# Performance work log

Measured on AMD Instinct MI355X. Metric: run time of the kernel, lower is better.

Reference implementation:

```python
import jax, jax.numpy as jnp
import numpy as np

HIDDEN = 1024
N_HEAD = 16
D_HEAD = HIDDEN // N_HEAD


def setup_inputs() -> dict:
    key = jax.random.key(0)
    k1, k2, k3, k4, k5, k6, k7 = jax.random.split(key, 7)
    B, Sq, Sk = 8, 1024, 1024
    decoder_input = jax.random.normal(k1, (B, Sq, HIDDEN), dtype=jnp.float32)
    encoder_output = jax.random.normal(k2, (B, Sk, HIDDEN), dtype=jnp.float32)
    # torch.rand -> uniform [0,1) for the per-head projection params
    W_query = jax.random.uniform(k3, (N_HEAD, D_HEAD, HIDDEN), dtype=jnp.float32)
    W_key = jax.random.uniform(k4, (N_HEAD, D_HEAD, HIDDEN), dtype=jnp.float32)
    W_value = jax.random.uniform(k5, (N_HEAD, D_HEAD, HIDDEN), dtype=jnp.float32)
    # nn.Linear default init: U(-1/sqrt(fan_in), 1/sqrt(fan_in))
    bound = 1.0 / np.sqrt(HIDDEN)
    W_out = jax.random.uniform(k6, (HIDDEN, HIDDEN), dtype=jnp.float32, minval=-bound, maxval=bound)
    b_out = jax.random.uniform(k7, (HIDDEN,), dtype=jnp.float32, minval=-bound, maxval=bound)
    return {
        "decoder_input": decoder_input,
        "encoder_output": encoder_output,
        "W_query": W_query,
        "W_key": W_key,
        "W_value": W_value,
        "W_out": W_out,
        "b_out": b_out,
    }


def reference(decoder_input, encoder_output, W_query, W_key, W_value, W_out, b_out):
    # per-head projections, vectorized over heads: x @ W[i].T == einsum over hidden
    q = jnp.einsum("bqh,ndh->bnqd", decoder_input, W_query)   # [B,N,Sq,D]
    k = jnp.einsum("bkh,ndh->bnkd", encoder_output, W_key)    # [B,N,Sk,D]
    v = jnp.einsum("bkh,ndh->bnkd", encoder_output, W_value)  # [B,N,Sk,D]
    scores = jnp.einsum("bnqd,bnkd->bnqk", q, k) / jnp.sqrt(jnp.float32(D_HEAD))
    attn = jax.nn.softmax(scores, axis=-1)                     # [B,N,Sq,Sk]
    heads = jnp.einsum("bnqk,bnkd->bnqd", attn, v)             # [B,N,Sq,D]
    B, N, Sq, D = heads.shape
    concat = jnp.transpose(heads, (0, 2, 1, 3)).reshape(B, Sq, N * D)  # [B,Sq,H]
    out = concat @ W_out.T + b_out
    return out
```

## Files before the change

### kernel.cpp

```cpp
#include <hip/hip_runtime.h>
#include <math.h>

#define HID 1024
#define NH 16
#define DH 64
#define BATCH 8
#define SEQ 1024
#define MTOT (BATCH * SEQ)

typedef __attribute__((ext_vector_type(8))) short bfrag;
typedef __attribute__((ext_vector_type(4))) float f32x4;
typedef __attribute__((ext_vector_type(8))) unsigned short us8;
typedef __attribute__((ext_vector_type(4))) unsigned short us4;
typedef unsigned int u32;
typedef unsigned short u16;

__device__ __forceinline__ u16 f2b(float f) {
    u32 u = __float_as_uint(f);
    return (u16)((u + 0x7FFFu + ((u >> 16) & 1u)) >> 16);
}
__device__ __forceinline__ float b2f(u16 h) { return __uint_as_float(((u32)h) << 16); }

__device__ __forceinline__ void gl_lds16(const void* g, void* l) {
    __builtin_amdgcn_global_load_lds(
        (const __attribute__((address_space(1))) unsigned int*)g,
        (__attribute__((address_space(3))) unsigned int*)l, 16, 0, 0);
}

__device__ __forceinline__ u32 swz(u32 L) { return L ^ (((L >> 6) & 7u) << 4); }
__device__ __forceinline__ u32 unswz(u32 p) {
    u32 b = ((((p >> 6) ^ (p >> 8)) & 1u) << 4) | (((p >> 7) & 1u) << 5) | (((p >> 8) & 1u) << 6);
    return p ^ b;
}

__global__ __launch_bounds__(256) void split_w(const float* __restrict__ x,
                                               u16* __restrict__ hi, u16* __restrict__ lo, int n4) {
    int i = blockIdx.x * blockDim.x + threadIdx.x;
    int stride = gridDim.x * blockDim.x;
    for (; i < n4; i += stride) {
        float4 f = ((const float4*)x)[i];
        float v[4] = {f.x, f.y, f.z, f.w};
        us4 h, l;
#pragma unroll
        for (int j = 0; j < 4; ++j) {
            u16 hh = f2b(v[j]);
            h[j] = hh;
            l[j] = f2b(v[j] - b2f(hh));
        }
        ((us4*)hi)[i] = h;
        ((us4*)lo)[i] = l;
    }
}
__global__ __launch_bounds__(256) void cvt_w(const float* __restrict__ x, u16* __restrict__ hi, int n4) {
    int i = blockIdx.x * blockDim.x + threadIdx.x;
    int stride = gridDim.x * blockDim.x;
    for (; i < n4; i += stride) {
        float4 f = ((const float4*)x)[i];
        us4 h;
        h[0] = f2b(f.x); h[1] = f2b(f.y); h[2] = f2b(f.z); h[3] = f2b(f.w);
        ((us4*)hi)[i] = h;
    }
}

template <int TERMS, int XMODE, int OMODE>
__global__ __launch_bounds__(256) void gemm_mfma(
    const float* __restrict__ Xf, const u16* __restrict__ Xb,
    const u16* __restrict__ Wh, const u16* __restrict__ Wl,
    const float* __restrict__ bias, float* __restrict__ Of, u16* __restrict__ Ob) {
    constexpr u32 OFF_AH = 0, OFF_BH = 8192, OFF_AL = 16384, OFF_BL = 24576;
    __shared__ __align__(16) char smem[(TERMS == 3) ? 32768 : 16384];

    u32 bid = blockIdx.x;
    u32 wg = (bid & 7) * 64 + (bid >> 3);
    const u32 m0 = (wg >> 3) * 128, n0 = (wg & 7) * 128;

    const int tid = threadIdx.x;
    const int w = tid >> 6, lane = tid & 63, c = lane & 15, g = lane >> 4;
    const int wr = w >> 1, wc = w & 1;

    u32 pa[4], pb[4];
#pragma unroll
    for (int i = 0; i < 4; ++i) {
        pa[i] = swz((u32)(wr * 64 + i * 16 + c) * 64 + (u32)g * 16);
        pb[i] = swz((u32)(wc * 64 + i * 16 + c) * 64 + (u32)g * 16);
    }

    f32x4 acc[4][4];
#pragma unroll
    for (int i = 0; i < 4; ++i)
#pragma unroll
        for (int j = 0; j < 4; ++j) acc[i][j] = f32x4{0.f, 0.f, 0.f, 0.f};

    for (int kb = 0; kb < HID / 32; ++kb) {
        const int koff = kb * 32;
        {
            const int nW = (TERMS == 3) ? 16 : 8;
            const int total = nW + ((XMODE == 1) ? 8 : 0);
            for (int id = w; id < total; id += 4) {
                u32 p = (u32)(id & 7) * 1024 + (u32)lane * 16;
                u32 L = unswz(p);
                u32 row = L >> 6, colb = L & 63;
                const char* src;
                u32 loff;
                if (id < 8) {
                    src = (const char*)Wh + ((size_t)(n0 + row)) * 2048 + (size_t)koff * 2 + colb;
                    loff = OFF_BH + (p & 0xFFFFFC00u);
                } else if (TERMS == 3 && id < 16) {
                    src = (const char*)Wl + ((size_t)(n0 + row)) * 2048 + (size_t)koff * 2 + colb;
                    loff = OFF_BL + (p & 0xFFFFFC00u);
                } else {
                    src = (const char*)Xb + ((size_t)(m0 + row)) * 2048 + (size_t)koff * 2 + colb;
                    loff = OFF_AH + (p & 0xFFFFFC00u);
                }
                gl_lds16(src, smem + loff);
            }
        }
        if (XMODE == 0) {
            const int row = tid >> 1, half = tid & 1;
            const float* xr = Xf + ((size_t)(m0 + row)) * HID + koff + half * 16;
            float4 f0 = ((const float4*)xr)[0], f1 = ((const float4*)xr)[1],
                   f2 = ((const float4*)xr)[2], f3 = ((const float4*)xr)[3];
            float v[16] = {f0.x, f0.y, f0.z, f0.w, f1.x, f1.y, f1.z, f1.w,
                           f2.x, f2.y, f2.z, f2.w, f3.x, f3.y, f3.z, f3.w};
#pragma unroll
            for (int s = 0; s < 2; ++s) {
                us8 h, l8;
#pragma unroll
                for (int i = 0; i < 8; ++i) {
                    u16 hh = f2b(v[s * 8 + i]);
                    h[i] = hh;
                    if (TERMS == 3) l8[i] = f2b(v[s * 8 + i] - b2f(hh));
                }
                u32 ph = swz((u32)row * 64 + (u32)half * 32 + (u32)s * 16);
                *(us8*)(smem + OFF_AH + ph) = h;
                if (TERMS == 3) *(us8*)(smem + OFF_AL + ph) = l8;
            }
        }
        __syncthreads();
        bfrag ah[4], al[4];
#pragma unroll
        for (int mi = 0; mi < 4; ++mi) {
            ah[mi] = *(const bfrag*)(smem + OFF_AH + pa[mi]);
            if (TERMS == 3) al[mi] = *(const bfrag*)(smem + OFF_AL + pa[mi]);
        }
#pragma unroll
        for (int ni = 0; ni < 4; ++ni) {
            bfrag bh = *(const bfrag*)(smem + OFF_BH + pb[ni]);
            bfrag bl;
            if (TERMS == 3) bl = *(const bfrag*)(smem + OFF_BL + pb[ni]);
#pragma unroll
            for (int mi = 0; mi < 4; ++mi) {
                acc[mi][ni] = __builtin_amdgcn_mfma_f32_16x16x32_bf16(ah[mi], bh, acc[mi][ni], 0, 0, 0);
                if (TERMS == 3) {
                    acc[mi][ni] = __builtin_amdgcn_mfma_f32_16x16x32_bf16(ah[mi], bl, acc[mi][ni], 0, 0, 0);
                    acc[mi][ni] = __builtin_amdgcn_mfma_f32_16x16x32_bf16(al[mi], bh, acc[mi][ni], 0, 0, 0);
                }
            }
        }
        __syncthreads();
    }
#pragma unroll
    for (int mi = 0; mi < 4; ++mi) {
#pragma unroll
        for (int ni = 0; ni < 4; ++ni) {
            const u32 n = n0 + wc * 64 + ni * 16 + c;
            float bv = (OMODE == 2) ? bias[n] : 0.f;
#pragma unroll
            for (int r = 0; r < 4; ++r) {
                const size_t m = m0 + wr * 64 + mi * 16 + 4 * g + r;
                float val = acc[mi][ni][r] + bv;
                if (OMODE == 1) Ob[m * HID + n] = f2b(val);
                else Of[m * HID + n] = val;
            }
        }
    }
}

__global__ __launch_bounds__(256) void attn_mfma(
    const float* __restrict__ Qf, const float* __restrict__ Kf,
    const u16* __restrict__ Vb, u16* __restrict__ Cc) {
    __shared__ __align__(16) u16 Qh[64 * 72], Ql[64 * 72], KP[64 * 72], KV[64 * 72];

    u32 bid = blockIdx.x;
    u32 wg = (bid & 7) * 256 + (bid >> 3);
    const int b = wg >> 8;
    const int head = (wg >> 4) & 15;
    const int q0 = (wg & 15) * 64;

    const int tid = threadIdx.x;
    const int w = tid >> 6, lane = tid & 63, c = lane & 15, g = lane >> 4;

    {
        const int row = tid >> 2, cs = tid & 3;
        const float* qr = Qf + ((size_t)(b * SEQ + q0 + row)) * HID + head * DH + cs * 16;
        float4 f0 = ((const float4*)qr)[0], f1 = ((const float4*)qr)[1],
               f2 = ((const float4*)qr)[2], f3 = ((const float4*)qr)[3];
        float v[16] = {f0.x, f0.y, f0.z, f0.w, f1.x, f1.y, f1.z, f1.w,
                       f2.x, f2.y, f2.z, f2.w, f3.x, f3.y, f3.z, f3.w};
#pragma unroll
        for (int s = 0; s < 2; ++s) {
            us8 h, l8;
#pragma unroll
            for (int i = 0; i < 8; ++i) {
                u16 hh = f2b(v[s * 8 + i]);
                h[i] = hh;
                l8[i] = f2b(v[s * 8 + i] - b2f(hh));
            }
            *(us8*)(Qh + row * 72 + cs * 16 + s * 8) = h;
            *(us8*)(Ql + row * 72 + cs * 16 + s * 8) = l8;
        }
    }

    float m_[4] = {-1e30f, -1e30f, -1e30f, -1e30f};
    float l_[4] = {0.f, 0.f, 0.f, 0.f};
    f32x4 acc[4];
#pragma unroll
    for (int j = 0; j < 4; ++j) acc[j] = f32x4{0.f, 0.f, 0.f, 0.f};

    for (int kc = 0; kc < SEQ / 64; ++kc) {
        __syncthreads();
        {
            const int row = tid >> 2, cs = tid & 3;
            const float* kr = Kf + ((size_t)(b * SEQ + kc * 64 + row)) * HID + head * DH + cs * 16;
            float4 f0 = ((const float4*)kr)[0], f1 = ((const float4*)kr)[1],
                   f2 = ((const float4*)kr)[2], f3 = ((const float4*)kr)[3];
            float v[16] = {f0.x, f0.y, f0.z, f0.w, f1.x, f1.y, f1.z, f1.w,
                           f2.x, f2.y, f2.z, f2.w, f3.x, f3.y, f3.z, f3.w};
#pragma unroll
            for (int s = 0; s < 2; ++s) {
                us8 h, l8;
#pragma unroll
                for (int i = 0; i < 8; ++i) {
                    u16 hh = f2b(v[s * 8 + i]);
                    h[i] = hh;
                    l8[i] = f2b(v[s * 8 + i] - b2f(hh));
                }
                *(us8*)(KP + row * 72 + cs * 16 + s * 8) = h;
                *(us8*)(KV + row * 72 + cs * 16 + s * 8) = l8;
            }
        }
        __syncthreads();
        f32x4 s4[4];
#pragma unroll
        for (int j = 0; j < 4; ++j) s4[j] = f32x4{0.f, 0.f, 0.f, 0.f};
#pragma unroll
        for (int ks = 0; ks < 2; ++ks) {
            bfrag ah = *(const bfrag*)(Qh + (w * 16 + c) * 72 + ks * 32 + g * 8);
            bfrag al = *(const bfrag*)(Ql + (w * 16 + c) * 72 + ks * 32 + g * 8);
#pragma unroll
            for (int jf = 0; jf < 4; ++jf) {
                bfrag bh = *(const bfrag*)(KP + (jf * 16 + c) * 72 + ks * 32 + g * 8);
                bfrag bl = *(const bfrag*)(KV + (jf * 16 + c) * 72 + ks * 32 + g * 8);
                s4[jf] = __builtin_amdgcn_mfma_f32_16x16x32_bf16(ah, bh, s4[jf], 0, 0, 0);
                s4[jf] = __builtin_amdgcn_mfma_f32_16x16x32_bf16(ah, bl, s4[jf], 0, 0, 0);
                s4[jf] = __builtin_amdgcn_mfma_f32_16x16x32_bf16(al, bh, s4[jf], 0, 0, 0);
            }
        }
        __syncthreads();
        float scl[4];
#pragma unroll
        for (int r = 0; r < 4; ++r) {
            float v0 = s4[0][r] * 0.125f, v1 = s4[1][r] * 0.125f,
                  v2 = s4[2][r] * 0.125f, v3 = s4[3][r] * 0.125f;
            float rm = fmaxf(fmaxf(v0, v1), fmaxf(v2, v3));
            rm = fmaxf(rm, __shfl_xor(rm, 1));
            rm = fmaxf(rm, __shfl_xor(rm, 2));
            rm = fmaxf(rm, __shfl_xor(rm, 4));
            rm = fmaxf(rm, __shfl_xor(rm, 8));
            float mn = fmaxf(m_[r], rm);
            scl[r] = __expf(m_[r] - mn);
            float p0 = __expf(v0 - mn), p1 = __expf(v1 - mn),
                  p2 = __expf(v2 - mn), p3 = __expf(v3 - mn);
            float rs = p0 + p1 + p2 + p3;
            rs += __shfl_xor(rs, 1);
            rs += __shfl_xor(rs, 2);
            rs += __shfl_xor(rs, 4);
            rs += __shfl_xor(rs, 8);
            l_[r] = l_[r] * scl[r] + rs;
            m_[r] = mn;
            const int prow = (w * 16 + 4 * g + r) * 72;
            KP[prow + 0 + c] = f2b(p0);
            KP[prow + 16 + c] = f2b(p1);
            KP[prow + 32 + c] = f2b(p2);
            KP[prow + 48 + c] = f2b(p3);
        }
#pragma unroll
        for (int jd = 0; jd < 4; ++jd) {
            f32x4 t = acc[jd];
            t[0] *= scl[0]; t[1] *= scl[1]; t[2] *= scl[2]; t[3] *= scl[3];
            acc[jd] = t;
        }
#pragma unroll
        for (int it = 0; it < 2; ++it) {
            const int idx = tid + it * 256;
            const int k = idx >> 3, ds = idx & 7, d0 = ds * 8;
            const u16* vr = Vb + ((size_t)(b * SEQ + kc * 64 + k)) * HID + head * DH + d0;
            us8 vv = *(const us8*)vr;
            const u32 kg = (((u32)(k >> 3)) ^ ((u32)ds & 3u)) << 3;
#pragma unroll
            for (int i = 0; i < 8; ++i) KV[(d0 + i) * 72 + kg + (k & 7)] = vv[i];
        }
        __syncthreads();
#pragma unroll
        for (int ks = 0; ks < 2; ++ks) {
            bfrag ap = *(const bfrag*)(KP + (w * 16 + c) * 72 + ks * 32 + g * 8);
#pragma unroll
            for (int jd = 0; jd < 4; ++jd) {
                const int d = jd * 16 + c;
                const u32 G = (u32)(ks * 4 + g);
                const u32 key = (u32)((d >> 3) & 3);
                bfrag bv = *(const bfrag*)(KV + d * 72 + ((G ^ key) << 3));
                acc[jd] = __builtin_amdgcn_mfma_f32_16x16x32_bf16(ap, bv, acc[jd], 0, 0, 0);
            }
        }
    }
    float inv[4] = {1.f / l_[0], 1.f / l_[1], 1.f / l_[2], 1.f / l_[3]};
#pragma unroll
    for (int jd = 0; jd < 4; ++jd) {
#pragma unroll
        for (int r = 0; r < 4; ++r) {
            Cc[((size_t)(b * SEQ + q0 + w * 16 + 4 * g + r)) * HID + head * DH + jd * 16 + c] =
                f2b(acc[jd][r] * inv[r]);
        }
    }
}

extern "C" void kernel_launch(void* const* d_in, const int* in_sizes, int n_in,
                              void* d_out, int out_size, void* d_ws, size_t ws_size,
                              hipStream_t stream) {
    const float* dec = (const float*)d_in[0];
    const float* enc = (const float*)d_in[1];
    const float* Wq = (const float*)d_in[2];
    const float* Wk = (const float*)d_in[3];
    const float* Wv = (const float*)d_in[4];
    const float* Wo = (const float*)d_in[5];
    const float* bo = (const float*)d_in[6];
    float* out = (float*)d_out;

    char* ws = (char*)d_ws;
    float* Qf = (float*)ws;
    float* Kf = (float*)(ws + (size_t)(32u << 20));
    u16* Vb = (u16*)(ws + (size_t)(64u << 20));
    u16* Cc = (u16*)(ws + (size_t)(80u << 20));
    u16* Wqh = (u16*)(ws + (size_t)(96u << 20));
    u16* Wql = Wqh + (1u << 20);
    u16* Wkh = Wql + (1u << 20);
    u16* Wkl = Wkh + (1u << 20);
    u16* Wvh = Wkl + (1u << 20);
    u16* Woh = Wvh + (1u << 20);

    const int n4w = HID * HID / 4;
    split_w<<<512, 256, 0, stream>>>(Wq, Wqh, Wql, n4w);
    split_w<<<512, 256, 0, stream>>>(Wk, Wkh, Wkl, n4w);
    cvt_w<<<512, 256, 0, stream>>>(Wv, Wvh, n4w);
    cvt_w<<<512, 256, 0, stream>>>(Wo, Woh, n4w);

    gemm_mfma<3, 0, 0><<<512, 256, 0, stream>>>(dec, nullptr, Wqh, Wql, nullptr, Qf, nullptr);
    gemm_mfma<3, 0, 0><<<512, 256, 0, stream>>>(enc, nullptr, Wkh, Wkl, nullptr, Kf, nullptr);
    gemm_mfma<1, 0, 1><<<512, 256, 0, stream>>>(enc, nullptr, Wvh, nullptr, nullptr, nullptr, Vb);

    attn_mfma<<<2048, 256, 0, stream>>>(Qf, Kf, Vb, Cc);

    gemm_mfma<1, 1, 2><<<512, 256, 0, stream>>>(nullptr, Cc, Woh, nullptr, bo, out, nullptr);
}
```

Before: 488.7 us.

## Emit head-major bf16 hi/lo Q/K and transposed V from projection epilogues

The Q and K projection epilogues now write bf16 hi/lo pairs in a [B,H,S,D] layout, with the softmax scale and log2e folded into Q. V is written pre-transposed as [B,H,D,S]. The attention kernel loads all tiles with direct global-to-LDS copies under an XOR swizzle, drops the per-tile fp32 split and V transpose, uses exp2, and removes two barriers per iteration. The weight conversion kernels are merged into one prep kernel, which also converts the encoder input to bf16 for the V GEMM. This cuts attention-side global traffic and ALU work, but adds strided scattered epilogue stores and an extra encoder conversion pass.

```diff
diff --git a/kernel.cpp b/kernel.cpp
--- a/kernel.cpp
+++ b/kernel.cpp
@@ -15,6 +15,8 @@
 typedef unsigned int u32;
 typedef unsigned short u16;
 
+#define SCALE_Q 0.18033688011112042f
+
 __device__ __forceinline__ u16 f2b(float f) {
     u32 u = __float_as_uint(f);
     return (u16)((u + 0x7FFFu + ((u >> 16) & 1u)) >> 16);
@@ -32,41 +34,55 @@
     u32 b = ((((p >> 6) ^ (p >> 8)) & 1u) << 4) | (((p >> 7) & 1u) << 5) | (((p >> 8) & 1u) << 6);
     return p ^ b;
 }
-
-__global__ __launch_bounds__(256) void split_w(const float* __restrict__ x,
-                                               u16* __restrict__ hi, u16* __restrict__ lo, int n4) {
-    int i = blockIdx.x * blockDim.x + threadIdx.x;
-    int stride = gridDim.x * blockDim.x;
-    for (; i < n4; i += stride) {
-        float4 f = ((const float4*)x)[i];
-        float v[4] = {f.x, f.y, f.z, f.w};
-        us4 h, l;
-#pragma unroll
-        for (int j = 0; j < 4; ++j) {
-            u16 hh = f2b(v[j]);
-            h[j] = hh;
-            l[j] = f2b(v[j] - b2f(hh));
-        }
-        ((us4*)hi)[i] = h;
-        ((us4*)lo)[i] = l;
-    }
-}
-__global__ __launch_bounds__(256) void cvt_w(const float* __restrict__ x, u16* __restrict__ hi, int n4) {
-    int i = blockIdx.x * blockDim.x + threadIdx.x;
-    int stride = gridDim.x * blockDim.x;
-    for (; i < n4; i += stride) {
-        float4 f = ((const float4*)x)[i];
-        us4 h;
-        h[0] = f2b(f.x); h[1] = f2b(f.y); h[2] = f2b(f.z); h[3] = f2b(f.w);
-        ((us4*)hi)[i] = h;
-    }
-}
-
-template <int TERMS, int XMODE, int OMODE>
+__device__ __forceinline__ u32 swz128(u32 L) { return L ^ (((L >> 7) & 7u) << 4); }
+
+__global__ __launch_bounds__(256) void prep(
+    const float* __restrict__ enc,
+    const float* __restrict__ Wq, const float* __restrict__ Wk,
+    const float* __restrict__ Wv, const float* __restrict__ Wo,
+    u16* __restrict__ Eh,
+    u16* __restrict__ Wqh, u16* __restrict__ Wql,
+    u16* __restrict__ Wkh, u16* __restrict__ Wkl,
+    u16* __restrict__ Wvh, u16* __restrict__ Woh)
+{
+    const int NX4 = MTOT * HID / 4;
+    const int NW4 = HID * HID / 4;
+    const int total = NX4 + 4 * NW4;
+    for (int i = blockIdx.x * blockDim.x + threadIdx.x; i < total;
+         i += gridDim.x * blockDim.x) {
+        if (i < NX4) {
+            float4 f = ((const float4*)enc)[i];
+            us4 h;
+            h[0] = f2b(f.x); h[1] = f2b(f.y); h[2] = f2b(f.z); h[3] = f2b(f.w);
+            ((us4*)Eh)[i] = h;
+        } else {
+            int j = i - NX4;
+            int rgn = j / NW4, k = j - rgn * NW4;
+            const float* src = (rgn == 0) ? Wq : (rgn == 1) ? Wk : (rgn == 2) ? Wv : Wo;
+            float4 f = ((const float4*)src)[k];
+            float v[4] = {f.x, f.y, f.z, f.w};
+            us4 h, l;
+#pragma unroll
+            for (int q = 0; q < 4; ++q) {
+                u16 hh = f2b(v[q]);
+                h[q] = hh;
+                l[q] = f2b(v[q] - b2f(hh));
+            }
+            if (rgn == 0) { ((us4*)Wqh)[k] = h; ((us4*)Wql)[k] = l; }
+            else if (rgn == 1) { ((us4*)Wkh)[k] = h; ((us4*)Wkl)[k] = l; }
+            else if (rgn == 2) { ((us4*)Wvh)[k] = h; }
+            else { ((us4*)Woh)[k] = h; }
+        }
+    }
+}
+
+template <int TERMS, int XMODE, int EPI>
 __global__ __launch_bounds__(256) void gemm_mfma(
     const float* __restrict__ Xf, const u16* __restrict__ Xb,
     const u16* __restrict__ Wh, const u16* __restrict__ Wl,
-    const float* __restrict__ bias, float* __restrict__ Of, u16* __restrict__ Ob) {
+    const float* __restrict__ bias, float scale,
+    float* __restrict__ Of, u16* __restrict__ O1, u16* __restrict__ O2)
+{
     constexpr u32 OFF_AH = 0, OFF_BH = 8192, OFF_AL = 16384, OFF_BL = 24576;
     __shared__ __align__(16) char smem[(TERMS == 3) ? 32768 : 16384];
 
@@ -94,8 +110,8 @@
     for (int kb = 0; kb < HID / 32; ++kb) {
         const int koff = kb * 32;
         {
-            const int nW = (TERMS == 3) ? 16 : 8;
-            const int total = nW + ((XMODE == 1) ? 8 : 0);
+            const int nB = (TERMS == 3) ? 16 : 8;
+            const int total = nB + ((XMODE == 1) ? 8 : 0);
             for (int id = w; id < total; id += 4) {
                 u32 p = (u32)(id & 7) * 1024 + (u32)lane * 16;
                 u32 L = unswz(p);
@@ -164,22 +180,42 @@
 #pragma unroll
         for (int ni = 0; ni < 4; ++ni) {
             const u32 n = n0 + wc * 64 + ni * 16 + c;
-            float bv = (OMODE == 2) ? bias[n] : 0.f;
-#pragma unroll
-            for (int r = 0; r < 4; ++r) {
-                const size_t m = m0 + wr * 64 + mi * 16 + 4 * g + r;
-                float val = acc[mi][ni][r] + bv;
-                if (OMODE == 1) Ob[m * HID + n] = f2b(val);
-                else Of[m * HID + n] = val;
+            const u32 mb = m0 + wr * 64 + mi * 16 + 4 * g;
+            if (EPI == 0) {
+                float bv = bias[n];
+#pragma unroll
+                for (int r = 0; r < 4; ++r)
+                    Of[(size_t)(mb + r) * HID + n] = acc[mi][ni][r] + bv;
+            } else if (EPI == 2) {
+                const u32 h = n >> 6, d = n & 63;
+                const u32 b_ = mb >> 10, s = mb & 1023;
+                size_t base = ((size_t)(b_ * NH + h) * SEQ + s) * 64 + d;
+#pragma unroll
+                for (int r = 0; r < 4; ++r) {
+                    float v = acc[mi][ni][r] * scale;
+                    u16 hh = f2b(v);
+                    O1[base + (size_t)r * 64] = hh;
+                    O2[base + (size_t)r * 64] = f2b(v - b2f(hh));
+                }
+            } else {
+                const u32 h = n >> 6, d = n & 63;
+                const u32 b_ = mb >> 10, s = mb & 1023;
+                us4 o;
+#pragma unroll
+                for (int r = 0; r < 4; ++r) o[r] = f2b(acc[mi][ni][r]);
+                *(us4*)&O1[((size_t)(b_ * NH + h) * 64 + d) * SEQ + s] = o;
             }
         }
     }
 }
 
 __global__ __launch_bounds__(256) void attn_mfma(
-    const float* __restrict__ Qf, const float* __restrict__ Kf,
-    const u16* __restrict__ Vb, u16* __restrict__ Cc) {
-    __shared__ __align__(16) u16 Qh[64 * 72], Ql[64 * 72], KP[64 * 72], KV[64 * 72];
+    const u16* __restrict__ Qh, const u16* __restrict__ Ql,
+    const u16* __restrict__ Kh, const u16* __restrict__ Kl,
+    const u16* __restrict__ Vt, u16* __restrict__ Cc)
+{
+    __shared__ __align__(16) u16 sQH[4096], sQL[4096], sKH[4096], sKL[4096], sVT[4096];
+    __shared__ __align__(16) u16 sP[64 * 72];
 
     u32 bid = blockIdx.x;
     u32 wg = (bid & 7) * 256 + (bid >> 3);
@@ -190,25 +226,20 @@
     const int tid = threadIdx.x;
     const int w = tid >> 6, lane = tid & 63, c = lane & 15, g = lane >> 4;
 
-    {
-        const int row = tid >> 2, cs = tid & 3;
-        const float* qr = Qf + ((size_t)(b * SEQ + q0 + row)) * HID + head * DH + cs * 16;
-        float4 f0 = ((const float4*)qr)[0], f1 = ((const float4*)qr)[1],
-               f2 = ((const float4*)qr)[2], f3 = ((const float4*)qr)[3];
-        float v[16] = {f0.x, f0.y, f0.z, f0.w, f1.x, f1.y, f1.z, f1.w,
-                       f2.x, f2.y, f2.z, f2.w, f3.x, f3.y, f3.z, f3.w};
-#pragma unroll
-        for (int s = 0; s < 2; ++s) {
-            us8 h, l8;
-#pragma unroll
-            for (int i = 0; i < 8; ++i) {
-                u16 hh = f2b(v[s * 8 + i]);
-                h[i] = hh;
-                l8[i] = f2b(v[s * 8 + i] - b2f(hh));
-            }
-            *(us8*)(Qh + row * 72 + cs * 16 + s * 8) = h;
-            *(us8*)(Ql + row * 72 + cs * 16 + s * 8) = l8;
-        }
+    const size_t hb = (size_t)(b * NH + head);
+    const char* gQH = (const char*)(Qh + (hb * SEQ + q0) * 64);
+    const char* gQL = (const char*)(Ql + (hb * SEQ + q0) * 64);
+    const char* gKH = (const char*)(Kh + hb * SEQ * 64);
+    const char* gKL = (const char*)(Kl + hb * SEQ * 64);
+    const char* gVT = (const char*)(Vt + hb * 64 * SEQ);
+
+    for (int t = w; t < 16; t += 4) {
+        u32 seg = (u32)(t & 7);
+        u32 p = seg * 1024 + (u32)lane * 16;
+        u32 ps = swz128(p);
+        const char* src = ((t < 8) ? gQH : gQL) + ps;
+        u16* dst = ((t < 8) ? sQH : sQL) + seg * 512;
+        gl_lds16(src, dst);
     }
 
     float m_[4] = {-1e30f, -1e30f, -1e30f, -1e30f};
@@ -219,58 +250,59 @@
 
     for (int kc = 0; kc < SEQ / 64; ++kc) {
         __syncthreads();
-        {
-            const int row = tid >> 2, cs = tid & 3;
-            const float* kr = Kf + ((size_t)(b * SEQ + kc * 64 + row)) * HID + head * DH + cs * 16;
-            float4 f0 = ((const float4*)kr)[0], f1 = ((const float4*)kr)[1],
-                   f2 = ((const float4*)kr)[2], f3 = ((const float4*)kr)[3];
-            float v[16] = {f0.x, f0.y, f0.z, f0.w, f1.x, f1.y, f1.z, f1.w,
-                           f2.x, f2.y, f2.z, f2.w, f3.x, f3.y, f3.z, f3.w};
-#pragma unroll
-            for (int s = 0; s < 2; ++s) {
-                us8 h, l8;
-#pragma unroll
-                for (int i = 0; i < 8; ++i) {
-                    u16 hh = f2b(v[s * 8 + i]);
-                    h[i] = hh;
-                    l8[i] = f2b(v[s * 8 + i] - b2f(hh));
-                }
-                *(us8*)(KP + row * 72 + cs * 16 + s * 8) = h;
-                *(us8*)(KV + row * 72 + cs * 16 + s * 8) = l8;
-            }
+        for (int t = w; t < 24; t += 4) {
+            u32 seg = (u32)(t & 7);
+            u32 p = seg * 1024 + (u32)lane * 16;
+            u32 ps = swz128(p);
+            const char* src;
+            u16* dst;
+            if (t < 8) {
+                src = gKH + (size_t)kc * 8192 + ps;
+                dst = sKH + seg * 512;
+            } else if (t < 16) {
+                src = gKL + (size_t)kc * 8192 + ps;
+                dst = sKL + seg * 512;
+            } else {
+                u32 row = ps >> 7, col = ps & 127;
+                src = gVT + (size_t)row * (SEQ * 2) + (size_t)kc * 128 + col;
+                dst = sVT + seg * 512;
+            }
+            gl_lds16(src, dst);
         }
         __syncthreads();
+
         f32x4 s4[4];
 #pragma unroll
         for (int j = 0; j < 4; ++j) s4[j] = f32x4{0.f, 0.f, 0.f, 0.f};
 #pragma unroll
         for (int ks = 0; ks < 2; ++ks) {
-            bfrag ah = *(const bfrag*)(Qh + (w * 16 + c) * 72 + ks * 32 + g * 8);
-            bfrag al = *(const bfrag*)(Ql + (w * 16 + c) * 72 + ks * 32 + g * 8);
+            u32 aoff = swz128((u32)(w * 16 + c) * 128 + (u32)ks * 64 + (u32)g * 16);
+            bfrag ah = *(const bfrag*)((const char*)sQH + aoff);
+            bfrag al = *(const bfrag*)((const char*)sQL + aoff);
 #pragma unroll
             for (int jf = 0; jf < 4; ++jf) {
-                bfrag bh = *(const bfrag*)(KP + (jf * 16 + c) * 72 + ks * 32 + g * 8);
-                bfrag bl = *(const bfrag*)(KV + (jf * 16 + c) * 72 + ks * 32 + g * 8);
+                u32 boff = swz128((u32)(jf * 16 + c) * 128 + (u32)ks * 64 + (u32)g * 16);
+                bfrag bh = *(const bfrag*)((const char*)sKH + boff);
+                bfrag bl = *(const bfrag*)((const char*)sKL + boff);
                 s4[jf] = __builtin_amdgcn_mfma_f32_16x16x32_bf16(ah, bh, s4[jf], 0, 0, 0);
                 s4[jf] = __builtin_amdgcn_mfma_f32_16x16x32_bf16(ah, bl, s4[jf], 0, 0, 0);
                 s4[jf] = __builtin_amdgcn_mfma_f32_16x16x32_bf16(al, bh, s4[jf], 0, 0, 0);
             }
         }
-        __syncthreads();
+
         float scl[4];
 #pragma unroll
         for (int r = 0; r < 4; ++r) {
-            float v0 = s4[0][r] * 0.125f, v1 = s4[1][r] * 0.125f,
-                  v2 = s4[2][r] * 0.125f, v3 = s4[3][r] * 0.125f;
+            float v0 = s4[0][r], v1 = s4[1][r], v2 = s4[2][r], v3 = s4[3][r];
             float rm = fmaxf(fmaxf(v0, v1), fmaxf(v2, v3));
             rm = fmaxf(rm, __shfl_xor(rm, 1));
             rm = fmaxf(rm, __shfl_xor(rm, 2));
             rm = fmaxf(rm, __shfl_xor(rm, 4));
             rm = fmaxf(rm, __shfl_xor(rm, 8));
             float mn = fmaxf(m_[r], rm);
-            scl[r] = __expf(m_[r] - mn);
-            float p0 = __expf(v0 - mn), p1 = __expf(v1 - mn),
-                  p2 = __expf(v2 - mn), p3 = __expf(v3 - mn);
+            scl[r] = exp2f(m_[r] - mn);
+            float p0 = exp2f(v0 - mn), p1 = exp2f(v1 - mn),
+                  p2 = exp2f(v2 - mn), p3 = exp2f(v3 - mn);
             float rs = p0 + p1 + p2 + p3;
             rs += __shfl_xor(rs, 1);
             rs += __shfl_xor(rs, 2);
@@ -279,10 +311,10 @@
             l_[r] = l_[r] * scl[r] + rs;
             m_[r] = mn;
             const int prow = (w * 16 + 4 * g + r) * 72;
-            KP[prow + 0 + c] = f2b(p0);
-            KP[prow + 16 + c] = f2b(p1);
-            KP[prow + 32 + c] = f2b(p2);
-            KP[prow + 48 + c] = f2b(p3);
+            sP[prow + 0 + c] = f2b(p0);
+            sP[prow + 16 + c] = f2b(p1);
+            sP[prow + 32 + c] = f2b(p2);
+            sP[prow + 48 + c] = f2b(p3);
         }
 #pragma unroll
         for (int jd = 0; jd < 4; ++jd) {
@@ -290,30 +322,19 @@
             t[0] *= scl[0]; t[1] *= scl[1]; t[2] *= scl[2]; t[3] *= scl[3];
             acc[jd] = t;
         }
-#pragma unroll
-        for (int it = 0; it < 2; ++it) {
-            const int idx = tid + it * 256;
-            const int k = idx >> 3, ds = idx & 7, d0 = ds * 8;
-            const u16* vr = Vb + ((size_t)(b * SEQ + kc * 64 + k)) * HID + head * DH + d0;
-            us8 vv = *(const us8*)vr;
-            const u32 kg = (((u32)(k >> 3)) ^ ((u32)ds & 3u)) << 3;
-#pragma unroll
-            for (int i = 0; i < 8; ++i) KV[(d0 + i) * 72 + kg + (k & 7)] = vv[i];
-        }
-        __syncthreads();
+
 #pragma unroll
         for (int ks = 0; ks < 2; ++ks) {
-            bfrag ap = *(const bfrag*)(KP + (w * 16 + c) * 72 + ks * 32 + g * 8);
+            bfrag ap = *(const bfrag*)(sP + (w * 16 + c) * 72 + ks * 32 + g * 8);
 #pragma unroll
             for (int jd = 0; jd < 4; ++jd) {
-                const int d = jd * 16 + c;
-                const u32 G = (u32)(ks * 4 + g);
-                const u32 key = (u32)((d >> 3) & 3);
-                bfrag bv = *(const bfrag*)(KV + d * 72 + ((G ^ key) << 3));
+                u32 voff = swz128((u32)(jd * 16 + c) * 128 + (u32)ks * 64 + (u32)g * 16);
+                bfrag bv = *(const bfrag*)((const char*)sVT + voff);
                 acc[jd] = __builtin_amdgcn_mfma_f32_16x16x32_bf16(ap, bv, acc[jd], 0, 0, 0);
             }
         }
     }
+
     float inv[4] = {1.f / l_[0], 1.f / l_[1], 1.f / l_[2], 1.f / l_[3]};
 #pragma unroll
     for (int jd = 0; jd < 4; ++jd) {
@@ -327,7 +348,8 @@
 
 extern "C" void kernel_launch(void* const* d_in, const int* in_sizes, int n_in,
                               void* d_out, int out_size, void* d_ws, size_t ws_size,
-                              hipStream_t stream) {
+                              hipStream_t stream)
+{
     const float* dec = (const float*)d_in[0];
     const float* enc = (const float*)d_in[1];
     const float* Wq = (const float*)d_in[2];
@@ -338,28 +360,33 @@
     float* out = (float*)d_out;
 
     char* ws = (char*)d_ws;
-    float* Qf = (float*)ws;
-    float* Kf = (float*)(ws + (size_t)(32u << 20));
-    u16* Vb = (u16*)(ws + (size_t)(64u << 20));
-    u16* Cc = (u16*)(ws + (size_t)(80u << 20));
-    u16* Wqh = (u16*)(ws + (size_t)(96u << 20));
+    const size_t MB = 1u << 20;
+    u16* Eh  = (u16*)ws;
+    u16* Qhg = (u16*)(ws + 16 * MB);
+    u16* Qlg = (u16*)(ws + 32 * MB);
+    u16* Khg = (u16*)(ws + 48 * MB);
+    u16* Klg = (u16*)(ws + 64 * MB);
+    u16* Vtg = (u16*)(ws + 80 * MB);
+    u16* Wqh = (u16*)(ws + 96 * MB);
     u16* Wql = Wqh + (1u << 20);
     u16* Wkh = Wql + (1u << 20);
     u16* Wkl = Wkh + (1u << 20);
     u16* Wvh = Wkl + (1u << 20);
     u16* Woh = Wvh + (1u << 20);
-
-    const int n4w = HID * HID / 4;
-    split_w<<<512, 256, 0, stream>>>(Wq, Wqh, Wql, n4w);
-    split_w<<<512, 256, 0, stream>>>(Wk, Wkh, Wkl, n4w);
-    cvt_w<<<512, 256, 0, stream>>>(Wv, Wvh, n4w);
-    cvt_w<<<512, 256, 0, stream>>>(Wo, Woh, n4w);
-
-    gemm_mfma<3, 0, 0><<<512, 256, 0, stream>>>(dec, nullptr, Wqh, Wql, nullptr, Qf, nullptr);
-    gemm_mfma<3, 0, 0><<<512, 256, 0, stream>>>(enc, nullptr, Wkh, Wkl, nullptr, Kf, nullptr);
-    gemm_mfma<1, 0, 1><<<512, 256, 0, stream>>>(enc, nullptr, Wvh, nullptr, nullptr, nullptr, Vb);
-
-    attn_mfma<<<2048, 256, 0, stream>>>(Qf, Kf, Vb, Cc);
-
-    gemm_mfma<1, 1, 2><<<512, 256, 0, stream>>>(nullptr, Cc, Woh, nullptr, bo, out, nullptr);
-}
+    u16* Cc  = Eh;
+
+    prep<<<2048, 256, 0, stream>>>(enc, Wq, Wk, Wv, Wo,
+                                   Eh, Wqh, Wql, Wkh, Wkl, Wvh, Woh);
+
+    gemm_mfma<3, 0, 2><<<512, 256, 0, stream>>>(dec, nullptr, Wqh, Wql, nullptr,
+                                                SCALE_Q, nullptr, Qhg, Qlg);
+    gemm_mfma<3, 0, 2><<<512, 256, 0, stream>>>(enc, nullptr, Wkh, Wkl, nullptr,
+                                                1.0f, nullptr, Khg, Klg);
+    gemm_mfma<1, 1, 3><<<512, 256, 0, stream>>>(nullptr, Eh, Wvh, nullptr, nullptr,
+                                                1.0f, nullptr, Vtg, nullptr);
+
+    attn_mfma<<<2048, 256, 0, stream>>>(Qhg, Qlg, Khg, Klg, Vtg, Cc);
+
+    gemm_mfma<1, 1, 0><<<512, 256, 0, stream>>>(nullptr, Cc, Woh, nullptr, bo,
+                                                1.0f, out, nullptr, nullptr);
+}
```

Measured after the change: 462.1 us. 5.4% less time.
